# Kernel tuning notes

Hardware: AMD Instinct MI355X
Metric: run time of the kernel (lower is better)

## Reference

```python
import jax, jax.numpy as jnp
import numpy as np

B, H, W, C = 4, 256, 256, 96
WIN = 8            # window size
HEADS = 3
HD = C // HEADS    # head dim = 32
SCALE = HD ** -0.5
N = WIN * WIN      # tokens per window = 64
HID = 4 * C        # MLP hidden


def _rel_pos_index(w):
    coords = np.stack(np.meshgrid(np.arange(w), np.arange(w), indexing='ij')).reshape(2, -1)
    rel = coords[:, :, None] - coords[:, None, :]         # (2, N, N)
    rel = rel.transpose(1, 2, 0).astype(np.int64)          # (N, N, 2)
    rel[:, :, 0] += w - 1
    rel[:, :, 1] += w - 1
    rel[:, :, 0] *= 2 * w - 1
    return jnp.asarray(rel.sum(-1))                        # (N, N)

REL_IDX = _rel_pos_index(WIN)


def layernorm(x, g, b, eps=1e-5):
    mu = jnp.mean(x, -1, keepdims=True)
    var = jnp.mean(jnp.square(x - mu), -1, keepdims=True)
    return (x - mu) * jax.lax.rsqrt(var + eps) * g + b


def setup_inputs() -> dict:
    key = jax.random.key(0)
    ks = jax.random.split(key, 8)
    s = 0.02
    return {
        'x': jax.random.normal(ks[0], (B, H, W, C), jnp.float32),
        'norm1_g': jnp.ones((C,), jnp.float32),
        'norm1_b': jnp.zeros((C,), jnp.float32),
        'qkv_w': jax.random.normal(ks[1], (C, 3 * C), jnp.float32) * s,
        'qkv_b': jnp.zeros((3 * C,), jnp.float32),
        'proj_w': jax.random.normal(ks[2], (C, C), jnp.float32) * s,
        'proj_b': jnp.zeros((C,), jnp.float32),
        'rel_bias_table': jax.random.normal(ks[3], ((2 * WIN - 1) ** 2, HEADS), jnp.float32) * s,
        'norm2_g': jnp.ones((C,), jnp.float32),
        'norm2_b': jnp.zeros((C,), jnp.float32),
        'fc1_w': jax.random.normal(ks[4], (C, HID), jnp.float32) * s,
        'fc1_b': jnp.zeros((HID,), jnp.float32),
        'fc2_w': jax.random.normal(ks[5], (HID, C), jnp.float32) * s,
        'fc2_b': jnp.zeros((C,), jnp.float32),
    }


def reference(x, norm1_g, norm1_b, qkv_w, qkv_b, proj_w, proj_b,
              rel_bias_table, norm2_g, norm2_b, fc1_w, fc1_b, fc2_w, fc2_b):
    shortcut = x
    h = layernorm(x, norm1_g, norm1_b)
    # window partition: (B,H,W,C) -> (B*nW, N, C)
    hw = h.reshape(B, H // WIN, WIN, W // WIN, WIN, C)
    hw = hw.transpose(0, 1, 3, 2, 4, 5).reshape(-1, N, C)
    Bw = hw.shape[0]
    # qkv projection
    qkv = hw @ qkv_w + qkv_b                               # (Bw, N, 3C)
    qkv = qkv.reshape(Bw, N, 3, HEADS, HD)
    q = jnp.transpose(qkv[:, :, 0], (0, 2, 1, 3))          # (Bw, h, N, d)
    k = jnp.transpose(qkv[:, :, 1], (0, 2, 1, 3))
    v = jnp.transpose(qkv[:, :, 2], (0, 2, 1, 3))
    attn = jnp.einsum('bhnd,bhmd->bhnm', q * SCALE, k)     # (Bw, h, N, N)
    bias = rel_bias_table[REL_IDX].transpose(2, 0, 1)      # (h, N, N)
    attn = jax.nn.softmax(attn + bias[None], axis=-1)
    out = jnp.einsum('bhnm,bhmd->bhnd', attn, v)
    out = out.transpose(0, 2, 1, 3).reshape(Bw, N, C)
    out = out @ proj_w + proj_b
    # window reverse: (B*nW, N, C) -> (B,H,W,C)
    out = out.reshape(B, H // WIN, W // WIN, WIN, WIN, C)
    out = out.transpose(0, 1, 3, 2, 4, 5).reshape(B, H, W, C)
    x = shortcut + out
    h2 = layernorm(x, norm2_g, norm2_b)
    mlp = jax.nn.gelu(h2 @ fc1_w + fc1_b, approximate=False) @ fc2_w + fc2_b
    return x + mlp
```

## Files before the change

### kernel.cpp

```cpp
#include <hip/hip_runtime.h>
#include <hip/hip_bf16.h>

#define NWIN 4096
#define SCALE 0.17677669529663687f

typedef __attribute__((ext_vector_type(8))) short bf16x8;
typedef __attribute__((ext_vector_type(4))) float f32x4;
typedef __attribute__((ext_vector_type(4))) unsigned short u16x4;
typedef __attribute__((ext_vector_type(8))) unsigned short u16x8;

__device__ __forceinline__ unsigned short f2bf(float f) {
    __hip_bfloat16 h = __float2bfloat16(f);
    return *reinterpret_cast<unsigned short*>(&h);
}
__device__ __forceinline__ f32x4 MF(bf16x8 a, bf16x8 b, f32x4 c) {
    return __builtin_amdgcn_mfma_f32_16x16x32_bf16(a, b, c, 0, 0, 0);
}
__device__ __forceinline__ bf16x8 LD8(const unsigned short* p) {
    return *reinterpret_cast<const bf16x8*>(p);
}

__global__ __launch_bounds__(512) void k_prep(
    const float* __restrict__ qkvw, const float* __restrict__ projw,
    const float* __restrict__ fc1w, const float* __restrict__ fc2w,
    unsigned short* __restrict__ ws)
{
    int i = blockIdx.x*512 + threadIdx.x;
    if (i >= 110592) return;
    if (i < 27648)      { int k = i/288,        n = i%288; ws[n*96 + k]         = f2bf(qkvw[i]); }
    else if (i < 36864) { int j = i-27648;  int k = j/96,  n = j%96;  ws[27648 + n*96 + k]  = f2bf(projw[j]); }
    else if (i < 73728) { int j = i-36864;  int k = j/384, n = j%384; ws[36864 + n*96 + k]  = f2bf(fc1w[j]); }
    else                { int j = i-73728;  int k = j/96,  n = j%96;  ws[73728 + n*384 + k] = f2bf(fc2w[j]); }
}

__global__ __launch_bounds__(512) void k_fused(
    const float* __restrict__ x,
    const float* __restrict__ n1g, const float* __restrict__ n1b,
    const float* __restrict__ qkv_b, const float* __restrict__ proj_b,
    const float* __restrict__ btab,
    const float* __restrict__ n2g, const float* __restrict__ n2b,
    const float* __restrict__ fc1b, const float* __restrict__ fc2b,
    const unsigned short* __restrict__ wbf, float* __restrict__ out)
{
    extern __shared__ char smem[];
    float*          s_res  = (float*)smem;
    unsigned short* s_a    = (unsigned short*)(smem + 25600);
    float*          s_bias = (float*)(smem + 38912);
    float*          s_s    = (float*)(smem + 41616);
    unsigned short* s_p    = (unsigned short*)(smem + 59024);
    unsigned short* s_q    = (unsigned short*)(smem + 68240);
    unsigned short* s_k    = (unsigned short*)(smem + 83600);
    unsigned short* s_vt   = (unsigned short*)(smem + 98960);
    unsigned short* s_h    = (unsigned short*)(smem + 68240);

    const int tid  = threadIdx.x;
    const int wid  = tid >> 6, lane = tid & 63, l16 = lane & 15, l4 = lane >> 4;
    const int wb   = blockIdx.x;
    const int b    = wb >> 10, wrem = wb & 1023, wy = wrem >> 5, wx = wrem & 31;
    const long base = ((long)(b*256 + wy*8)*256 + (long)(wx*8))*96;
    const int mtile = wid >> 1;
    const int nh    = wid & 1;

    for (int i = tid; i < 64*24; i += 512) {
        int tok = i / 24, seg = i % 24;
        const float4 v = *reinterpret_cast<const float4*>(
            x + base + (long)(((tok >> 3) << 8) + (tok & 7))*96 + seg*4);
        *reinterpret_cast<float4*>(s_res + tok*100 + seg*4) = v;
    }
    for (int i = tid; i < 675; i += 512) s_bias[i] = btab[i];
    __syncthreads();

    {
        const int tok = tid >> 3, part = tid & 7;
        const float* rp = s_res + tok*100 + part*12;
        float4 v0 = *reinterpret_cast<const float4*>(rp);
        float4 v1 = *reinterpret_cast<const float4*>(rp + 4);
        float4 v2 = *reinterpret_cast<const float4*>(rp + 8);
        float r[12] = {v0.x,v0.y,v0.z,v0.w, v1.x,v1.y,v1.z,v1.w, v2.x,v2.y,v2.z,v2.w};
        float s1 = 0.f, s2 = 0.f;
        #pragma unroll
        for (int i = 0; i < 12; ++i) { s1 += r[i]; s2 += r[i]*r[i]; }
        s1 += __shfl_xor(s1,1); s2 += __shfl_xor(s2,1);
        s1 += __shfl_xor(s1,2); s2 += __shfl_xor(s2,2);
        s1 += __shfl_xor(s1,4); s2 += __shfl_xor(s2,4);
        float mu = s1*(1.f/96.f), var = s2*(1.f/96.f) - mu*mu;
        float rs = rsqrtf(var + 1e-5f);
        unsigned short* wp = s_a + tok*104 + part*12;
        #pragma unroll
        for (int q = 0; q < 3; ++q) {
            u16x4 pk;
            #pragma unroll
            for (int j = 0; j < 4; ++j) {
                int c = part*12 + q*4 + j;
                pk[j] = f2bf((r[q*4+j]-mu)*rs*n1g[c] + n1b[c]);
            }
            *reinterpret_cast<u16x4*>(wp + q*4) = pk;
        }
    }
    __syncthreads();

    {
        const unsigned short* ap = s_a + (mtile*16 + l16)*104 + l4*8;
        const bf16x8 a0 = LD8(ap), a1 = LD8(ap+32), a2 = LD8(ap+64);
        #pragma unroll
        for (int u = 0; u < 9; ++u) {
            const int ntile = nh*9 + u;
            const unsigned short* bp = wbf + (ntile*16 + l16)*96 + l4*8;
            f32x4 acc = {0.f,0.f,0.f,0.f};
            acc = MF(a0, LD8(bp),    acc);
            acc = MF(a1, LD8(bp+32), acc);
            acc = MF(a2, LD8(bp+64), acc);
            const int col = ntile*16 + l16;
            const float bv = qkv_b[col];
            const int sel = col/96, hc = col%96, h = hc >> 5, d = hc & 31;
            if (sel < 2) {
                unsigned short* q = (sel == 0 ? s_q : s_k) + h*2560 + d;
                #pragma unroll
                for (int r = 0; r < 4; ++r)
                    q[(mtile*16 + l4*4 + r)*40] = f2bf(acc[r] + bv);
            } else {
                u16x4 pk;
                #pragma unroll
                for (int r = 0; r < 4; ++r) pk[r] = f2bf(acc[r] + bv);
                *reinterpret_cast<u16x4*>(s_vt + h*2304 + d*72 + mtile*16 + l4*4) = pk;
            }
        }
    }
    __syncthreads();

    for (int h = 0; h < 3; ++h) {
        {
            const unsigned short* ap = s_q + h*2560 + (mtile*16 + l16)*40 + l4*8;
            const bf16x8 af = LD8(ap);
            #pragma unroll
            for (int u = 0; u < 2; ++u) {
                const int ntile = nh*2 + u;
                const unsigned short* bp = s_k + h*2560 + (ntile*16 + l16)*40 + l4*8;
                f32x4 acc = {0.f,0.f,0.f,0.f};
                acc = MF(af, LD8(bp), acc);
                const int col = ntile*16 + l16;
                const int yj = col >> 3, xj = col & 7;
                #pragma unroll
                for (int r = 0; r < 4; ++r) {
                    const int row = mtile*16 + l4*4 + r;
                    const int yi = row >> 3, xi = row & 7;
                    const int ridx = (yi-yj+7)*15 + (xi-xj+7);
                    s_s[row*68 + col] = acc[r]*SCALE + s_bias[ridx*3 + h];
                }
            }
        }
        if (h > 0) {
            const unsigned short* ap = s_p + (mtile*16 + l16)*72 + l4*8;
            const bf16x8 a0 = LD8(ap), a1 = LD8(ap+32);
            const unsigned short* bp = s_vt + (h-1)*2304 + (nh*16 + l16)*72 + l4*8;
            f32x4 acc = {0.f,0.f,0.f,0.f};
            acc = MF(a0, LD8(bp),    acc);
            acc = MF(a1, LD8(bp+32), acc);
            #pragma unroll
            for (int r = 0; r < 4; ++r)
                s_a[(mtile*16 + l4*4 + r)*104 + (h-1)*32 + nh*16 + l16] = f2bf(acc[r]);
        }
        __syncthreads();
        {
            const int i = tid >> 3, part = tid & 7;
            const float* sp = s_s + i*68 + part*8;
            float4 v0 = *reinterpret_cast<const float4*>(sp);
            float4 v1 = *reinterpret_cast<const float4*>(sp + 4);
            float v[8] = {v0.x,v0.y,v0.z,v0.w, v1.x,v1.y,v1.z,v1.w};
            float m = v[0];
            #pragma unroll
            for (int u = 1; u < 8; ++u) m = fmaxf(m, v[u]);
            m = fmaxf(m, __shfl_xor(m,1)); m = fmaxf(m, __shfl_xor(m,2)); m = fmaxf(m, __shfl_xor(m,4));
            float s = 0.f;
            #pragma unroll
            for (int u = 0; u < 8; ++u) { v[u] = __expf(v[u] - m); s += v[u]; }
            s += __shfl_xor(s,1); s += __shfl_xor(s,2); s += __shfl_xor(s,4);
            const float inv = 1.f/s;
            u16x8 pk;
            #pragma unroll
            for (int u = 0; u < 8; ++u) pk[u] = f2bf(v[u]*inv);
            *reinterpret_cast<u16x8*>(s_p + i*72 + part*8) = pk;
        }
        __syncthreads();
    }
    {
        const unsigned short* ap = s_p + (mtile*16 + l16)*72 + l4*8;
        const bf16x8 a0 = LD8(ap), a1 = LD8(ap+32);
        const unsigned short* bp = s_vt + 2*2304 + (nh*16 + l16)*72 + l4*8;
        f32x4 acc = {0.f,0.f,0.f,0.f};
        acc = MF(a0, LD8(bp),    acc);
        acc = MF(a1, LD8(bp+32), acc);
        #pragma unroll
        for (int r = 0; r < 4; ++r)
            s_a[(mtile*16 + l4*4 + r)*104 + 2*32 + nh*16 + l16] = f2bf(acc[r]);
    }
    __syncthreads();

    {
        const unsigned short* ap = s_a + (mtile*16 + l16)*104 + l4*8;
        const bf16x8 a0 = LD8(ap), a1 = LD8(ap+32), a2 = LD8(ap+64);
        #pragma unroll
        for (int u = 0; u < 3; ++u) {
            const int ntile = nh*3 + u;
            const unsigned short* bp = wbf + 27648 + (ntile*16 + l16)*96 + l4*8;
            f32x4 acc = {0.f,0.f,0.f,0.f};
            acc = MF(a0, LD8(bp),    acc);
            acc = MF(a1, LD8(bp+32), acc);
            acc = MF(a2, LD8(bp+64), acc);
            const int c = ntile*16 + l16;
            const float pb = proj_b[c];
            #pragma unroll
            for (int r = 0; r < 4; ++r) {
                const int tok = mtile*16 + l4*4 + r;
                s_res[tok*100 + c] += acc[r] + pb;
            }
        }
    }
    __syncthreads();

    {
        const int tok = tid >> 3, part = tid & 7;
        const float* rp = s_res + tok*100 + part*12;
        float4 v0 = *reinterpret_cast<const float4*>(rp);
        float4 v1 = *reinterpret_cast<const float4*>(rp + 4);
        float4 v2 = *reinterpret_cast<const float4*>(rp + 8);
        float r[12] = {v0.x,v0.y,v0.z,v0.w, v1.x,v1.y,v1.z,v1.w, v2.x,v2.y,v2.z,v2.w};
        float s1 = 0.f, s2 = 0.f;
        #pragma unroll
        for (int i = 0; i < 12; ++i) { s1 += r[i]; s2 += r[i]*r[i]; }
        s1 += __shfl_xor(s1,1); s2 += __shfl_xor(s2,1);
        s1 += __shfl_xor(s1,2); s2 += __shfl_xor(s2,2);
        s1 += __shfl_xor(s1,4); s2 += __shfl_xor(s2,4);
        float mu = s1*(1.f/96.f), var = s2*(1.f/96.f) - mu*mu;
        float rs = rsqrtf(var + 1e-5f);
        unsigned short* wp = s_a + tok*104 + part*12;
        #pragma unroll
        for (int q = 0; q < 3; ++q) {
            u16x4 pk;
            #pragma unroll
            for (int j = 0; j < 4; ++j) {
                int c = part*12 + q*4 + j;
                pk[j] = f2bf((r[q*4+j]-mu)*rs*n2g[c] + n2b[c]);
            }
            *reinterpret_cast<u16x4*>(wp + q*4) = pk;
        }
    }
    __syncthreads();

    f32x4 macc[3];
    #pragma unroll
    for (int u = 0; u < 3; ++u) macc[u] = (f32x4){0.f,0.f,0.f,0.f};

    for (int ch = 0; ch < 2; ++ch) {
        {
            const unsigned short* ap = s_a + (mtile*16 + l16)*104 + l4*8;
            const bf16x8 a0 = LD8(ap), a1 = LD8(ap+32), a2 = LD8(ap+64);
            #pragma unroll
            for (int u = 0; u < 6; ++u) {
                const int ntile = nh*6 + u;
                const int hcol = ntile*16 + l16;
                const unsigned short* bp = wbf + 36864 + (ch*192 + hcol)*96 + l4*8;
                f32x4 acc = {0.f,0.f,0.f,0.f};
                acc = MF(a0, LD8(bp),    acc);
                acc = MF(a1, LD8(bp+32), acc);
                acc = MF(a2, LD8(bp+64), acc);
                const float fb = fc1b[ch*192 + hcol];
                #pragma unroll
                for (int r = 0; r < 4; ++r) {
                    float v = acc[r] + fb;
                    float g = v / (1.f + __expf(-1.5957691216057308f*(v + 0.044715f*v*v*v)));
                    s_h[(mtile*16 + l4*4 + r)*200 + hcol] = f2bf(g);
                }
            }
        }
        __syncthreads();
        {
            const unsigned short* ap = s_h + (mtile*16 + l16)*200 + l4*8;
            bf16x8 af[6];
            #pragma unroll
            for (int kc = 0; kc < 6; ++kc) af[kc] = LD8(ap + kc*32);
            #pragma unroll
            for (int u = 0; u < 3; ++u) {
                const int n = (nh*3 + u)*16 + l16;
                const unsigned short* bp = wbf + 73728 + n*384 + ch*192 + l4*8;
                #pragma unroll
                for (int kc = 0; kc < 6; ++kc)
                    macc[u] = MF(af[kc], LD8(bp + kc*32), macc[u]);
            }
        }
        if (ch == 0) __syncthreads();
    }

    {
        #pragma unroll
        for (int u = 0; u < 3; ++u) {
            const int c = (nh*3 + u)*16 + l16;
            const float fb = fc2b[c];
            #pragma unroll
            for (int r = 0; r < 4; ++r) {
                const int tok = mtile*16 + l4*4 + r;
                out[base + (long)(((tok >> 3) << 8) + (tok & 7))*96 + c] =
                    s_res[tok*100 + c] + macc[u][r] + fb;
            }
        }
    }
}

extern "C" void kernel_launch(void* const* d_in, const int* in_sizes, int n_in,
                              void* d_out, int out_size, void* d_ws, size_t ws_size,
                              hipStream_t stream) {
    (void)in_sizes; (void)n_in; (void)out_size; (void)ws_size;
    const float* x     = (const float*)d_in[0];
    const float* n1g   = (const float*)d_in[1];
    const float* n1b   = (const float*)d_in[2];
    const float* qkvw  = (const float*)d_in[3];
    const float* qkvb  = (const float*)d_in[4];
    const float* projw = (const float*)d_in[5];
    const float* projb = (const float*)d_in[6];
    const float* btab  = (const float*)d_in[7];
    const float* n2g   = (const float*)d_in[8];
    const float* n2b   = (const float*)d_in[9];
    const float* fc1w  = (const float*)d_in[10];
    const float* fc1b  = (const float*)d_in[11];
    const float* fc2w  = (const float*)d_in[12];
    const float* fc2b  = (const float*)d_in[13];
    float* out = (float*)d_out;
    unsigned short* ws = (unsigned short*)d_ws;

    hipFuncSetAttribute(reinterpret_cast<const void*>(k_fused),
                        hipFuncAttributeMaxDynamicSharedMemorySize, 112784);

    k_prep<<<dim3(216), dim3(512), 0, stream>>>(qkvw, projw, fc1w, fc2w, ws);
    k_fused<<<dim3(NWIN), dim3(512), 112784, stream>>>(
        x, n1g, n1b, qkvb, projb, btab, n2g, n2b, fc1b, fc2b, ws, out);
}
```

Measured before the change: 595.6 us.

## Stage QKV, proj and MLP weights into padded LDS before each GEMM

Each GEMM stage now first copies its bf16 weight block from global memory into padded shared-memory buffers, then reads the MFMA B operands from LDS instead of issuing direct global loads. QKV weights are loaded alongside the input tile. Proj weights are loaded during head 0 of the attention loop. The fc1 and fc2 chunks are loaded at the start of each MLP chunk, and the padding is meant to avoid bank conflicts. The aim is to stop the four M-tile waves from each fetching the same weights from cache. The cost is extra copy work, an extra barrier per MLP chunk, and shared memory growing to nearly the full 160KB per CU.

After: 486.5 us. -18.3%, faster.

```diff
diff --git a/kernel.cpp b/kernel.cpp
--- a/kernel.cpp
+++ b/kernel.cpp
@@ -45,13 +45,15 @@
     extern __shared__ char smem[];
     float*          s_res  = (float*)smem;
     unsigned short* s_a    = (unsigned short*)(smem + 25600);
-    float*          s_bias = (float*)(smem + 38912);
-    float*          s_s    = (float*)(smem + 41616);
-    unsigned short* s_p    = (unsigned short*)(smem + 59024);
-    unsigned short* s_q    = (unsigned short*)(smem + 68240);
-    unsigned short* s_k    = (unsigned short*)(smem + 83600);
-    unsigned short* s_vt   = (unsigned short*)(smem + 98960);
-    unsigned short* s_h    = (unsigned short*)(smem + 68240);
+    unsigned short* s_w    = (unsigned short*)(smem + 38912);
+    float*          s_s    = (float*)(smem + 61584);
+    unsigned short* s_p    = (unsigned short*)(smem + 78992);
+    unsigned short* s_q    = (unsigned short*)(smem + 98816);
+    unsigned short* s_k    = (unsigned short*)(smem + 114176);
+    unsigned short* s_vt   = (unsigned short*)(smem + 129536);
+    float*          s_bias = (float*)(smem + 143360);
+    unsigned short* s_h    = (unsigned short*)(smem + 98816);
+    unsigned short* s_w2   = (unsigned short*)(smem + 124416);
 
     const int tid  = threadIdx.x;
     const int wid  = tid >> 6, lane = tid & 63, l16 = lane & 15, l4 = lane >> 4;
@@ -68,6 +70,14 @@
         *reinterpret_cast<float4*>(s_res + tok*100 + seg*4) = v;
     }
     for (int i = tid; i < 675; i += 512) s_bias[i] = btab[i];
+    {
+        uint4* dst = reinterpret_cast<uint4*>(s_w);
+        const uint4* src = reinterpret_cast<const uint4*>(wbf);
+        for (int i = tid; i < 288*12; i += 512) {
+            int r = i / 12, sg = i % 12;
+            dst[r*13 + sg] = src[r*12 + sg];
+        }
+    }
     __syncthreads();
 
     {
@@ -105,7 +115,7 @@
         #pragma unroll
         for (int u = 0; u < 9; ++u) {
             const int ntile = nh*9 + u;
-            const unsigned short* bp = wbf + (ntile*16 + l16)*96 + l4*8;
+            const unsigned short* bp = s_w + (ntile*16 + l16)*104 + l4*8;
             f32x4 acc = {0.f,0.f,0.f,0.f};
             acc = MF(a0, LD8(bp),    acc);
             acc = MF(a1, LD8(bp+32), acc);
@@ -149,7 +159,14 @@
                 }
             }
         }
-        if (h > 0) {
+        if (h == 0) {
+            uint4* dst = reinterpret_cast<uint4*>(s_w);
+            const uint4* src = reinterpret_cast<const uint4*>(wbf) + 3456;
+            for (int i = tid; i < 96*12; i += 512) {
+                int r = i/12, sg = i%12;
+                dst[r*13 + sg] = src[r*12 + sg];
+            }
+        } else {
             const unsigned short* ap = s_p + (mtile*16 + l16)*72 + l4*8;
             const bf16x8 a0 = LD8(ap), a1 = LD8(ap+32);
             const unsigned short* bp = s_vt + (h-1)*2304 + (nh*16 + l16)*72 + l4*8;
@@ -202,7 +219,7 @@
         #pragma unroll
         for (int u = 0; u < 3; ++u) {
             const int ntile = nh*3 + u;
-            const unsigned short* bp = wbf + 27648 + (ntile*16 + l16)*96 + l4*8;
+            const unsigned short* bp = s_w + (ntile*16 + l16)*104 + l4*8;
             f32x4 acc = {0.f,0.f,0.f,0.f};
             acc = MF(a0, LD8(bp),    acc);
             acc = MF(a1, LD8(bp+32), acc);
@@ -245,7 +262,6 @@
             *reinterpret_cast<u16x4*>(wp + q*4) = pk;
         }
     }
-    __syncthreads();
 
     f32x4 macc[3];
     #pragma unroll
@@ -253,13 +269,27 @@
 
     for (int ch = 0; ch < 2; ++ch) {
         {
+            uint4* d1 = reinterpret_cast<uint4*>(s_w);
+            uint4* d2 = reinterpret_cast<uint4*>(s_w2);
+            const uint4* src = reinterpret_cast<const uint4*>(wbf);
+            for (int i = tid; i < 192*12; i += 512) {
+                int r = i/12, sg = i%12;
+                d1[r*13 + sg] = src[4608 + (ch*192 + r)*12 + sg];
+            }
+            for (int i = tid; i < 96*24; i += 512) {
+                int n = i/24, sg = i%24;
+                d2[n*25 + sg] = src[9216 + n*48 + ch*24 + sg];
+            }
+        }
+        __syncthreads();
+        {
             const unsigned short* ap = s_a + (mtile*16 + l16)*104 + l4*8;
             const bf16x8 a0 = LD8(ap), a1 = LD8(ap+32), a2 = LD8(ap+64);
             #pragma unroll
             for (int u = 0; u < 6; ++u) {
                 const int ntile = nh*6 + u;
                 const int hcol = ntile*16 + l16;
-                const unsigned short* bp = wbf + 36864 + (ch*192 + hcol)*96 + l4*8;
+                const unsigned short* bp = s_w + hcol*104 + l4*8;
                 f32x4 acc = {0.f,0.f,0.f,0.f};
                 acc = MF(a0, LD8(bp),    acc);
                 acc = MF(a1, LD8(bp+32), acc);
@@ -281,14 +311,13 @@
             for (int kc = 0; kc < 6; ++kc) af[kc] = LD8(ap + kc*32);
             #pragma unroll
             for (int u = 0; u < 3; ++u) {
-                const int n = (nh*3 + u)*16 + l16;
-                const unsigned short* bp = wbf + 73728 + n*384 + ch*192 + l4*8;
+                const unsigned short* bp = s_w2 + ((nh*3 + u)*16 + l16)*200 + l4*8;
                 #pragma unroll
                 for (int kc = 0; kc < 6; ++kc)
                     macc[u] = MF(af[kc], LD8(bp + kc*32), macc[u]);
             }
         }
-        if (ch == 0) __syncthreads();
+        __syncthreads();
     }
 
     {
@@ -328,9 +357,9 @@
     unsigned short* ws = (unsigned short*)d_ws;
 
     hipFuncSetAttribute(reinterpret_cast<const void*>(k_fused),
-                        hipFuncAttributeMaxDynamicSharedMemorySize, 112784);
+                        hipFuncAttributeMaxDynamicSharedMemorySize, 162816);
 
     k_prep<<<dim3(216), dim3(512), 0, stream>>>(qkvw, projw, fc1w, fc2w, ws);
-    k_fused<<<dim3(NWIN), dim3(512), 112784, stream>>>(
+    k_fused<<<dim3(NWIN), dim3(512), 162816, stream>>>(
         x, n1g, n1b, qkvb, projb, btab, n2g, n2b, fc1b, fc2b, ws, out);
 }
```
